# Kernel tuning notes

Hardware: AMD Instinct MI355X
Metric: run time of the kernel (lower is better)

The kernel has to match this reference:

```python
import jax, jax.numpy as jnp
import numpy as np

KN = 4        # kernel_number
K = 3         # kernel size
CIN = 256
COUT = 256
BN_EPS = 1e-5


def _rotation_matrices(thetas):
    """thetas: [b, n] -> rot mats [b, n, 9, 9] (faithful port of _get_rotation_matrix)."""
    b, n = thetas.shape
    t = thetas.reshape(-1)                      # [b*n]
    x = jnp.cos(t); y = jnp.sin(t)
    a = x - y; bxy = x * y; c = x + y
    z = jnp.zeros_like(t); o = jnp.ones_like(t)
    pos = [
        [a, 1 - a, z, z, z, z, z, z, z],
        [z, x - bxy, bxy, z, 1 - c + bxy, y - bxy, z, z, z],
        [z, z, a, z, z, 1 - a, z, z, z],
        [bxy, y - bxy, z, x - bxy, 1 - c + bxy, z, z, z, z],
        [z, z, z, z, o, z, z, z, z],
        [z, z, z, z, 1 - c + bxy, x - bxy, z, y - bxy, bxy],
        [z, z, z, 1 - a, z, z, a, z, z],
        [z, z, z, y - bxy, 1 - c + bxy, z, bxy, x - bxy, z],
        [z, z, z, z, z, z, z, 1 - a, a],
    ]
    neg = [
        [c, z, z, 1 - c, z, z, z, z, z],
        [-bxy, x + bxy, z, bxy - y, 1 - a - bxy, z, z, z, z],
        [z, 1 - c, c, z, z, z, z, z, z],
        [z, z, z, x + bxy, 1 - a - bxy, z, -bxy, bxy - y, z],
        [z, z, z, z, o, z, z, z, z],
        [z, bxy - y, -bxy, z, 1 - a - bxy, x + bxy, z, z, z],
        [z, z, z, z, z, z, c, 1 - c, z],
        [z, z, z, z, 1 - a - bxy, bxy - y, z, x + bxy, -bxy],
        [z, z, z, z, z, 1 - c, z, z, c],
    ]
    P = jnp.stack([jnp.stack(r, 0) for r in pos], 0)    # [9, 9, b*n]
    N = jnp.stack([jnp.stack(r, 0) for r in neg], 0)    # [9, 9, b*n]
    R = jnp.where(t >= 0, P, N)                          # [9, 9, b*n]
    return R.transpose(2, 0, 1).reshape(b, n, K * K, K * K)


def _rotate_weights(weights, lambdas, thetas):
    """weights [n, Cout, Cin, 3, 3], lambdas/thetas [b, n] -> [b*Cout, Cin, 3, 3]."""
    b, n = thetas.shape
    _, Cout, Cin, _, _ = weights.shape
    rot = _rotation_matrices(thetas) * lambdas[:, :, None, None]   # [b, n, 9, 9]
    rot = rot.transpose(0, 2, 1, 3).reshape(b * K * K, n * K * K)  # [b*9, n*9]
    w = weights.transpose(0, 3, 4, 1, 2).reshape(n * K * K, Cout * Cin)
    w = rot @ w                                                    # [b*9, Cout*Cin]
    w = w.reshape(b, K, K, Cout, Cin).transpose(0, 3, 4, 1, 2)
    return w.reshape(b * Cout, Cin, K, K)


def _forward(x, weight, w_lambda, w_theta, bn_gamma, bn_beta, bn_mean, bn_var):
    b, Cin, H, W = x.shape
    Cout = weight.shape[1]
    # routing: GAP -> linear heads (sigmoid for lambdas, softsign*pi for thetas)
    pooled = x.mean(axis=(2, 3))                        # [b, Cin]
    lambdas = jax.nn.sigmoid(pooled @ w_lambda)         # [b, n]
    thetas = jax.nn.soft_sign(pooled @ w_theta) * jnp.pi  # [b, n]
    # per-sample rotated weights + grouped conv (groups = b)
    rw = _rotate_weights(weight, lambdas, thetas)       # [b*Cout, Cin, 3, 3]
    xr = x.reshape(1, b * Cin, H, W)
    out = jax.lax.conv_general_dilated(
        xr, rw, window_strides=(1, 1), padding=((1, 1), (1, 1)),
        dimension_numbers=('NCHW', 'OIHW', 'NCHW'), feature_group_count=b)
    out = out.reshape(b, Cout, H, W)
    # BatchNorm (inference, running stats) + ReLU
    inv = jax.lax.rsqrt(bn_var + BN_EPS)
    out = (out - bn_mean[None, :, None, None]) * (inv * bn_gamma)[None, :, None, None] \
          + bn_beta[None, :, None, None]
    return jax.nn.relu(out)


def setup_inputs() -> dict:
    key = jax.random.key(0)
    ks = jax.random.split(key, 8)
    B, H, W = 16, 64, 64
    x = jax.random.normal(ks[0], (B, CIN, H, W), dtype=jnp.float32)
    fan_in = CIN * K * K
    weight = jax.random.normal(ks[1], (KN, COUT, CIN, K, K), dtype=jnp.float32) * np.sqrt(2.0 / fan_in)
    w_lambda = jax.random.normal(ks[2], (CIN, KN), dtype=jnp.float32) * np.sqrt(2.0 / CIN)
    w_theta = jax.random.normal(ks[3], (CIN, KN), dtype=jnp.float32) * np.sqrt(2.0 / CIN)
    bn_gamma = jax.random.uniform(ks[4], (COUT,), dtype=jnp.float32, minval=0.5, maxval=1.5)
    bn_beta = jax.random.normal(ks[5], (COUT,), dtype=jnp.float32) * 0.1
    bn_mean = jax.random.normal(ks[6], (COUT,), dtype=jnp.float32) * 0.1
    bn_var = jax.random.uniform(ks[7], (COUT,), dtype=jnp.float32, minval=0.5, maxval=1.5)
    return {'x': x, 'weight': weight, 'w_lambda': w_lambda, 'w_theta': w_theta,
            'bn_gamma': bn_gamma, 'bn_beta': bn_beta, 'bn_mean': bn_mean, 'bn_var': bn_var}


def reference(x, weight, w_lambda, w_theta, bn_gamma, bn_beta, bn_mean, bn_var):
    return _forward(x, weight, w_lambda, w_theta, bn_gamma, bn_beta, bn_mean, bn_var)
```

## Files before the change

### kernel.cpp

```cpp
#include <hip/hip_runtime.h>
#include <math.h>

#define B_   16
#define CIN_ 256
#define COUT_ 256
#define HW_  64
#define KN_  4

typedef __bf16  bf16x8 __attribute__((ext_vector_type(8)));
typedef float   f32x4  __attribute__((ext_vector_type(4)));

__global__ __launch_bounds__(256) void pool_kernel(const float* __restrict__ x,
                                                   float* __restrict__ pooled) {
    int bc = blockIdx.x;
    const float* p = x + (size_t)bc * 4096;
    int t = threadIdx.x;
    float s = 0.f;
#pragma unroll
    for (int i = 0; i < 16; i++) s += p[t + i * 256];
#pragma unroll
    for (int off = 32; off > 0; off >>= 1) s += __shfl_down(s, off, 64);
    __shared__ float red[4];
    if ((t & 63) == 0) red[t >> 6] = s;
    __syncthreads();
    if (t == 0) pooled[bc] = (red[0] + red[1] + red[2] + red[3]) * (1.f / 4096.f);
}

__global__ __launch_bounds__(256) void routing_kernel(
    const float* __restrict__ pooled,
    const float* __restrict__ w_lambda, const float* __restrict__ w_theta,
    const float* __restrict__ bn_gamma, const float* __restrict__ bn_beta,
    const float* __restrict__ bn_mean,  const float* __restrict__ bn_var,
    float* __restrict__ S, float* __restrict__ bnscale, float* __restrict__ bnshift) {
    int t = threadIdx.x;
    if (t < 256) {
        float inv = rsqrtf(bn_var[t] + 1e-5f);
        float sc = bn_gamma[t] * inv;
        bnscale[t] = sc;
        bnshift[t] = bn_beta[t] - bn_mean[t] * sc;
    }
    if (t < 64) {
        int b = t >> 2, n = t & 3;
        float zl = 0.f, zt = 0.f;
        for (int ci = 0; ci < 256; ci++) {
            float p = pooled[b * 256 + ci];
            zl += p * w_lambda[ci * 4 + n];
            zt += p * w_theta[ci * 4 + n];
        }
        float lam = 1.f / (1.f + expf(-zl));
        float th  = 3.14159265358979323846f * (zt / (1.f + fabsf(zt)));
        float xc = cosf(th), ys = sinf(th);
        float a = xc - ys, bb = xc * ys, c = xc + ys;
        float R[9][9];
#pragma unroll
        for (int i = 0; i < 9; i++)
#pragma unroll
            for (int j = 0; j < 9; j++) R[i][j] = 0.f;
        if (th >= 0.f) {
            R[0][0] = a;       R[0][1] = 1 - a;
            R[1][1] = xc - bb; R[1][2] = bb;       R[1][4] = 1 - c + bb; R[1][5] = ys - bb;
            R[2][2] = a;       R[2][5] = 1 - a;
            R[3][0] = bb;      R[3][1] = ys - bb;  R[3][3] = xc - bb;    R[3][4] = 1 - c + bb;
            R[4][4] = 1.f;
            R[5][4] = 1 - c + bb; R[5][5] = xc - bb; R[5][7] = ys - bb;  R[5][8] = bb;
            R[6][3] = 1 - a;   R[6][6] = a;
            R[7][3] = ys - bb; R[7][4] = 1 - c + bb; R[7][6] = bb;       R[7][7] = xc - bb;
            R[8][7] = 1 - a;   R[8][8] = a;
        } else {
            R[0][0] = c;       R[0][3] = 1 - c;
            R[1][0] = -bb;     R[1][1] = xc + bb;  R[1][3] = bb - ys;    R[1][4] = 1 - a - bb;
            R[2][1] = 1 - c;   R[2][2] = c;
            R[3][3] = xc + bb; R[3][4] = 1 - a - bb; R[3][6] = -bb;      R[3][7] = bb - ys;
            R[4][4] = 1.f;
            R[5][1] = bb - ys; R[5][2] = -bb;      R[5][4] = 1 - a - bb; R[5][5] = xc + bb;
            R[6][6] = c;       R[6][7] = 1 - c;
            R[7][4] = 1 - a - bb; R[7][5] = bb - ys; R[7][7] = xc + bb;  R[7][8] = -bb;
            R[8][5] = 1 - c;   R[8][8] = c;
        }
        float* Sp = S + (b * 4 + n) * 81;
#pragma unroll
        for (int p = 0; p < 9; p++)
#pragma unroll
            for (int q = 0; q < 9; q++) Sp[p * 9 + q] = lam * R[p][q];
    }
}

__global__ __launch_bounds__(256) void rotw_kernel(const float* __restrict__ weight,
                                                   const float* __restrict__ S,
                                                   __bf16* __restrict__ rwq) {
    __shared__ float sl[324];
    int b = blockIdx.y;
    int t = threadIdx.x;
    for (int i = t; i < 324; i += 256) sl[i] = S[b * 324 + i];
    __syncthreads();
    int flat = blockIdx.x * 256 + t;
    int co = flat >> 8, ci = flat & 255;
    float wv[4][9];
#pragma unroll
    for (int n = 0; n < 4; n++) {
        const float* wp = weight + (((size_t)n * 256 + co) * 256 + ci) * 9;
#pragma unroll
        for (int q = 0; q < 9; q++) wv[n][q] = wp[q];
    }
#pragma unroll
    for (int p = 0; p < 9; p++) {
        float s = 0.f;
#pragma unroll
        for (int n = 0; n < 4; n++) {
            const float* sp = sl + n * 81 + p * 9;
#pragma unroll
            for (int q = 0; q < 9; q++) s += sp[q] * wv[n][q];
        }
        rwq[(((size_t)b * 9 + p) * 256 + co) * 256 + ci] = (__bf16)s;
    }
}

__global__ __launch_bounds__(256, 3) void conv_kernel(
    const float* __restrict__ x, const __bf16* __restrict__ rwq,
    const float* __restrict__ bnscale, const float* __restrict__ bnshift,
    float* __restrict__ out) {
    __shared__ __attribute__((aligned(16))) __bf16 xs[6][66][40];
    __shared__ __attribute__((aligned(16))) __bf16 as3[3][64][40];

    const int t   = threadIdx.x;
    const int lane = t & 63;
    const int wv  = t >> 6;
    const int l15 = lane & 15;
    const int kq  = lane >> 4;

    const int h0  = blockIdx.x * 4;
    const int co0 = blockIdx.y * 64;
    const int b   = blockIdx.z;

    f32x4 acc[4][4];
#pragma unroll
    for (int m = 0; m < 4; m++)
#pragma unroll
        for (int n = 0; n < 4; n++) acc[m][n] = (f32x4){0.f, 0.f, 0.f, 0.f};

    if (t < 192) {
        int rr = t / 32, c = t % 32;
        xs[rr][0][c]  = (__bf16)0.f;
        xs[rr][65][c] = (__bf16)0.f;
    }

    for (int ci0 = 0; ci0 < 256; ci0 += 32) {
        __syncthreads();
#pragma unroll
        for (int i = 0; i < 12; i++) {
            int v    = t + i * 256;
            int w4   = v & 15;
            int pair = v >> 4;
            int rr   = pair >> 5;
            int c    = pair & 31;
            int hh   = h0 - 1 + rr;
            float4 val = {0.f, 0.f, 0.f, 0.f};
            if (hh >= 0 && hh < 64)
                val = *(const float4*)(x + (((size_t)(b * 256 + ci0 + c) * 64 + hh) * 64 + w4 * 4));
            int colb = w4 * 4 + 1;
            xs[rr][colb + 0][c] = (__bf16)val.x;
            xs[rr][colb + 1][c] = (__bf16)val.y;
            xs[rr][colb + 2][c] = (__bf16)val.z;
            xs[rr][colb + 3][c] = (__bf16)val.w;
        }
        for (int dh = 0; dh < 3; dh++) {
            __syncthreads();
#pragma unroll
            for (int j = 0; j < 3; j++) {
                int u   = t + j * 256;
                int dw  = u >> 8;
                int rem = u & 255;
                int co  = rem >> 2;
                int p8  = (rem & 3) * 8;
                const __bf16* src = rwq +
                    ((((size_t)b * 9 + dh * 3 + dw) * 256 + co0 + co) * 256 + ci0 + p8);
                *(uint4*)&as3[dw][co][p8] = *(const uint4*)src;
            }
            __syncthreads();
#pragma unroll
            for (int dw = 0; dw < 3; dw++) {
                bf16x8 af[4];
#pragma unroll
                for (int m = 0; m < 4; m++)
                    af[m] = *(const bf16x8*)&as3[dw][m * 16 + l15][kq * 8];
#pragma unroll
                for (int nt = 0; nt < 4; nt++) {
                    bf16x8 bfr = *(const bf16x8*)&xs[wv + dh][nt * 16 + l15 + dw][kq * 8];
#pragma unroll
                    for (int m = 0; m < 4; m++)
                        acc[m][nt] = __builtin_amdgcn_mfma_f32_16x16x32_bf16(
                            af[m], bfr, acc[m][nt], 0, 0, 0);
                }
            }
        }
    }

    const int h = h0 + wv;
#pragma unroll
    for (int m = 0; m < 4; m++) {
#pragma unroll
        for (int reg = 0; reg < 4; reg++) {
            int co = co0 + m * 16 + kq * 4 + reg;
            float sc = bnscale[co], sh = bnshift[co];
#pragma unroll
            for (int nt = 0; nt < 4; nt++) {
                int w = nt * 16 + l15;
                float v = acc[m][nt][reg] * sc + sh;
                out[(((size_t)b * 256 + co) * 64 + h) * 64 + w] = v > 0.f ? v : 0.f;
            }
        }
    }
}

extern "C" void kernel_launch(void* const* d_in, const int* in_sizes, int n_in,
                              void* d_out, int out_size, void* d_ws, size_t ws_size,
                              hipStream_t stream) {
    const float* x        = (const float*)d_in[0];
    const float* weight   = (const float*)d_in[1];
    const float* w_lambda = (const float*)d_in[2];
    const float* w_theta  = (const float*)d_in[3];
    const float* bn_gamma = (const float*)d_in[4];
    const float* bn_beta  = (const float*)d_in[5];
    const float* bn_mean  = (const float*)d_in[6];
    const float* bn_var   = (const float*)d_in[7];
    float* out = (float*)d_out;

    char* ws = (char*)d_ws;
    float*  pooled  = (float*)(ws);
    float*  S       = (float*)(ws + 16384);
    float*  bnscale = (float*)(ws + 40960);
    float*  bnshift = (float*)(ws + 45056);
    __bf16* rwq     = (__bf16*)(ws + 49152);

    pool_kernel<<<4096, 256, 0, stream>>>(x, pooled);
    routing_kernel<<<1, 256, 0, stream>>>(pooled, w_lambda, w_theta,
                                          bn_gamma, bn_beta, bn_mean, bn_var,
                                          S, bnscale, bnshift);
    rotw_kernel<<<dim3(256, 16), 256, 0, stream>>>(weight, S, rwq);
    conv_kernel<<<dim3(16, 4, 16), 256, 0, stream>>>(x, rwq, bnscale, bnshift, out);
}
```

Measured before the change: 281.1 us.

## Pre-transpose x to channel-last bf16 and stage conv tiles via global_load_lds

Adds a transpose kernel that converts x to a bf16 NHWC-like layout. The conv kernel can then fill LDS with direct 16-byte global-to-LDS loads for both activations and rotated weights, replacing the per-element fp32 conversion and scattered LDS stores. The LDS layout is re-tiled to [k-quarter][row][8] and occupancy is raised to 4 blocks per CU. rotw is also restructured to load each output channel's weights once into LDS and loop over the batch, reading S from global memory. The cost is an extra pass over x that writes a 32MB intermediate, and the new LDS layout may introduce bank conflicts.

```diff
diff --git a/kernel.cpp b/kernel.cpp
--- a/kernel.cpp
+++ b/kernel.cpp
@@ -1,14 +1,13 @@
 #include <hip/hip_runtime.h>
 #include <math.h>
 
-#define B_   16
-#define CIN_ 256
-#define COUT_ 256
-#define HW_  64
-#define KN_  4
-
 typedef __bf16  bf16x8 __attribute__((ext_vector_type(8)));
 typedef float   f32x4  __attribute__((ext_vector_type(4)));
+
+#define GLD_LDS16(dst, src)                                                      \
+    __builtin_amdgcn_global_load_lds(                                            \
+        (const __attribute__((address_space(1))) unsigned int*)(src),            \
+        (__attribute__((address_space(3))) unsigned int*)(dst), 16, 0, 0)
 
 __global__ __launch_bounds__(256) void pool_kernel(const float* __restrict__ x,
                                                    float* __restrict__ pooled) {
@@ -24,6 +23,21 @@
     if ((t & 63) == 0) red[t >> 6] = s;
     __syncthreads();
     if (t == 0) pooled[bc] = (red[0] + red[1] + red[2] + red[3]) * (1.f / 4096.f);
+}
+
+__global__ __launch_bounds__(256) void transpose_kernel(const float* __restrict__ x,
+                                                        __bf16* __restrict__ xT) {
+    int h = blockIdx.x, b = blockIdx.y;
+    int lane = threadIdx.x & 63, wv = threadIdx.x >> 6;
+#pragma unroll
+    for (int i = 0; i < 8; i++) {
+        int cq = i * 4 + wv;
+        const float* src = x + (((size_t)(b * 256 + cq * 8) * 64 + h) * 64 + lane);
+        bf16x8 o;
+#pragma unroll
+        for (int j = 0; j < 8; j++) o[j] = (__bf16)src[(size_t)j * 4096];
+        *(bf16x8*)(xT + (((size_t)(b * 64 + h) * 64 + lane) * 256 + cq * 8)) = o;
+    }
 }
 
 __global__ __launch_bounds__(256) void routing_kernel(
@@ -88,45 +102,48 @@
 __global__ __launch_bounds__(256) void rotw_kernel(const float* __restrict__ weight,
                                                    const float* __restrict__ S,
                                                    __bf16* __restrict__ rwq) {
-    __shared__ float sl[324];
-    int b = blockIdx.y;
+    __shared__ float wlds[4][2304];
+    int co = blockIdx.x;
     int t = threadIdx.x;
-    for (int i = t; i < 324; i += 256) sl[i] = S[b * 324 + i];
+#pragma unroll
+    for (int n = 0; n < 4; n++) {
+        const float* wp = weight + ((size_t)n * 256 + co) * 2304;
+        for (int i = t; i < 2304; i += 256) wlds[n][i] = wp[i];
+    }
     __syncthreads();
-    int flat = blockIdx.x * 256 + t;
-    int co = flat >> 8, ci = flat & 255;
-    float wv[4][9];
-#pragma unroll
-    for (int n = 0; n < 4; n++) {
-        const float* wp = weight + (((size_t)n * 256 + co) * 256 + ci) * 9;
-#pragma unroll
-        for (int q = 0; q < 9; q++) wv[n][q] = wp[q];
-    }
-#pragma unroll
-    for (int p = 0; p < 9; p++) {
-        float s = 0.f;
-#pragma unroll
-        for (int n = 0; n < 4; n++) {
-            const float* sp = sl + n * 81 + p * 9;
-#pragma unroll
-            for (int q = 0; q < 9; q++) s += sp[q] * wv[n][q];
-        }
-        rwq[(((size_t)b * 9 + p) * 256 + co) * 256 + ci] = (__bf16)s;
-    }
-}
-
-__global__ __launch_bounds__(256, 3) void conv_kernel(
-    const float* __restrict__ x, const __bf16* __restrict__ rwq,
+    int ci = t;
+    float w[4][9];
+#pragma unroll
+    for (int n = 0; n < 4; n++)
+#pragma unroll
+        for (int q = 0; q < 9; q++) w[n][q] = wlds[n][ci * 9 + q];
+    for (int b = 0; b < 16; b++) {
+#pragma unroll
+        for (int p = 0; p < 9; p++) {
+            float s = 0.f;
+#pragma unroll
+            for (int n = 0; n < 4; n++) {
+                const float* sp = S + (b * 4 + n) * 81 + p * 9;
+#pragma unroll
+                for (int q = 0; q < 9; q++) s += sp[q] * w[n][q];
+            }
+            rwq[(((size_t)b * 9 + p) * 256 + co) * 256 + ci] = (__bf16)s;
+        }
+    }
+}
+
+__global__ __launch_bounds__(256, 4) void conv_kernel(
+    const __bf16* __restrict__ xT, const __bf16* __restrict__ rwq,
     const float* __restrict__ bnscale, const float* __restrict__ bnshift,
     float* __restrict__ out) {
-    __shared__ __attribute__((aligned(16))) __bf16 xs[6][66][40];
-    __shared__ __attribute__((aligned(16))) __bf16 as3[3][64][40];
-
-    const int t   = threadIdx.x;
+    __shared__ __attribute__((aligned(16))) __bf16 xs[6][4][66][8];
+    __shared__ __attribute__((aligned(16))) __bf16 as3[3][4][64][8];
+
+    const int t    = threadIdx.x;
     const int lane = t & 63;
-    const int wv  = t >> 6;
-    const int l15 = lane & 15;
-    const int kq  = lane >> 4;
+    const int wv   = t >> 6;
+    const int l15  = lane & 15;
+    const int kq4  = lane >> 4;
 
     const int h0  = blockIdx.x * 4;
     const int co0 = blockIdx.y * 64;
@@ -139,42 +156,33 @@
         for (int n = 0; n < 4; n++) acc[m][n] = (f32x4){0.f, 0.f, 0.f, 0.f};
 
     if (t < 192) {
-        int rr = t / 32, c = t % 32;
-        xs[rr][0][c]  = (__bf16)0.f;
-        xs[rr][65][c] = (__bf16)0.f;
-    }
+        int rr = t / 32, kq = (t % 32) >> 3, j = t & 7;
+        xs[rr][kq][0][j]  = (__bf16)0.f;
+        xs[rr][kq][65][j] = (__bf16)0.f;
+    }
+    const uint4 zero4 = {0u, 0u, 0u, 0u};
 
     for (int ci0 = 0; ci0 < 256; ci0 += 32) {
         __syncthreads();
 #pragma unroll
-        for (int i = 0; i < 12; i++) {
-            int v    = t + i * 256;
-            int w4   = v & 15;
-            int pair = v >> 4;
-            int rr   = pair >> 5;
-            int c    = pair & 31;
-            int hh   = h0 - 1 + rr;
-            float4 val = {0.f, 0.f, 0.f, 0.f};
-            if (hh >= 0 && hh < 64)
-                val = *(const float4*)(x + (((size_t)(b * 256 + ci0 + c) * 64 + hh) * 64 + w4 * 4));
-            int colb = w4 * 4 + 1;
-            xs[rr][colb + 0][c] = (__bf16)val.x;
-            xs[rr][colb + 1][c] = (__bf16)val.y;
-            xs[rr][colb + 2][c] = (__bf16)val.z;
-            xs[rr][colb + 3][c] = (__bf16)val.w;
+        for (int u = wv * 6; u < wv * 6 + 6; u++) {
+            int rr = u >> 2, kq = u & 3;
+            int hh = h0 - 1 + rr;
+            if (hh >= 0 && hh < 64) {
+                const __bf16* src = xT + (((size_t)(b * 64 + hh) * 64 + lane) * 256 + ci0 + kq * 8);
+                GLD_LDS16(&xs[rr][kq][1 + lane][0], src);
+            } else {
+                *(uint4*)&xs[rr][kq][1 + lane][0] = zero4;
+            }
         }
         for (int dh = 0; dh < 3; dh++) {
             __syncthreads();
 #pragma unroll
-            for (int j = 0; j < 3; j++) {
-                int u   = t + j * 256;
-                int dw  = u >> 8;
-                int rem = u & 255;
-                int co  = rem >> 2;
-                int p8  = (rem & 3) * 8;
+            for (int u = wv * 3; u < wv * 3 + 3; u++) {
+                int dw = u >> 2, kq = u & 3;
                 const __bf16* src = rwq +
-                    ((((size_t)b * 9 + dh * 3 + dw) * 256 + co0 + co) * 256 + ci0 + p8);
-                *(uint4*)&as3[dw][co][p8] = *(const uint4*)src;
+                    ((((size_t)b * 9 + dh * 3 + dw) * 256 + co0 + lane) * 256 + ci0 + kq * 8);
+                GLD_LDS16(&as3[dw][kq][lane][0], src);
             }
             __syncthreads();
 #pragma unroll
@@ -182,10 +190,10 @@
                 bf16x8 af[4];
 #pragma unroll
                 for (int m = 0; m < 4; m++)
-                    af[m] = *(const bf16x8*)&as3[dw][m * 16 + l15][kq * 8];
+                    af[m] = *(const bf16x8*)&as3[dw][kq4][m * 16 + l15][0];
 #pragma unroll
                 for (int nt = 0; nt < 4; nt++) {
-                    bf16x8 bfr = *(const bf16x8*)&xs[wv + dh][nt * 16 + l15 + dw][kq * 8];
+                    bf16x8 bfr = *(const bf16x8*)&xs[wv + dh][kq4][nt * 16 + l15 + dw][0];
 #pragma unroll
                     for (int m = 0; m < 4; m++)
                         acc[m][nt] = __builtin_amdgcn_mfma_f32_16x16x32_bf16(
@@ -200,7 +208,7 @@
     for (int m = 0; m < 4; m++) {
 #pragma unroll
         for (int reg = 0; reg < 4; reg++) {
-            int co = co0 + m * 16 + kq * 4 + reg;
+            int co = co0 + m * 16 + kq4 * 4 + reg;
             float sc = bnscale[co], sh = bnshift[co];
 #pragma unroll
             for (int nt = 0; nt < 4; nt++) {
@@ -230,12 +238,14 @@
     float*  S       = (float*)(ws + 16384);
     float*  bnscale = (float*)(ws + 40960);
     float*  bnshift = (float*)(ws + 45056);
-    __bf16* rwq     = (__bf16*)(ws + 49152);
+    __bf16* xT      = (__bf16*)(ws + 49152);
+    __bf16* rwq     = (__bf16*)(ws + 49152 + 33554432);
 
     pool_kernel<<<4096, 256, 0, stream>>>(x, pooled);
+    transpose_kernel<<<dim3(64, 16), 256, 0, stream>>>(x, xT);
     routing_kernel<<<1, 256, 0, stream>>>(pooled, w_lambda, w_theta,
                                           bn_gamma, bn_beta, bn_mean, bn_var,
                                           S, bnscale, bnshift);
-    rotw_kernel<<<dim3(256, 16), 256, 0, stream>>>(weight, S, rwq);
-    conv_kernel<<<dim3(16, 4, 16), 256, 0, stream>>>(x, rwq, bnscale, bnshift, out);
-}
+    rotw_kernel<<<256, 256, 0, stream>>>(weight, S, rwq);
+    conv_kernel<<<dim3(16, 4, 16), 256, 0, stream>>>(xT, rwq, bnscale, bnshift, out);
+}
```

New measurement: 321.6 us. 1.14x slower.
